# Kernel optimization log

Measured on AMD Instinct MI355X. Metric: run time of the kernel, lower is better.

The kernel has to match this reference:

```python
import jax, jax.numpy as jnp
import numpy as np

RADIUS = 0.1
NSAMPLE = 64
NEVENT = 2048
B, N, D = 4, 16384, 62
CHANNEL = D + 2  # 64


def index_events(events, idx):
    # events: [B, N, C], idx: [B, ...] -> [B, ..., C]
    return jax.vmap(lambda e, i: e[i])(events, idx)


def square_distance(src, dst):
    # src: [B, S, 2], dst: [B, N, 2] -> [B, S, N]
    return (jnp.sum(src ** 2, -1)[:, :, None]
            + jnp.sum(dst ** 2, -1)[:, None, :]
            - 2.0 * jnp.einsum('bsc,bnc->bsn', src, dst))


def research_circle(radius, nsample, xy, new_xy):
    n = xy.shape[1]
    sqrdists = square_distance(new_xy, xy)            # [B, S, N]
    ar = jnp.arange(n, dtype=jnp.int32)
    group_idx = jnp.where(sqrdists > radius ** 2, n, ar)  # out-of-ball -> N (sorts last)
    group_idx = jnp.sort(group_idx, axis=-1)[:, :, :nsample]
    first = group_idx[:, :, :1]
    return jnp.where(group_idx == n, first, group_idx)     # [B, S, nsample]


def reference(xy, events, fps_idx, affine_alpha, affine_beta):
    b, _, c = xy.shape
    new_xy = index_events(xy, fps_idx)                     # [B, S, 2]
    idx = research_circle(RADIUS, NSAMPLE, xy, new_xy)     # [B, S, K]
    grouped_xy = index_events(xy, idx)                     # [B, S, K, 2]
    grouped_events = index_events(events, idx)             # [B, S, K, D]
    # Normalize (normalize='center')
    g = jnp.concatenate([grouped_events, grouped_xy], axis=-1)  # [B, S, K, D+2]
    mean = jnp.mean(g, axis=2, keepdims=True)              # [B, S, 1, C]
    centered = g - mean
    std = jnp.std(centered.reshape(b, -1), axis=-1, ddof=1)[:, None, None, None]
    g = centered / (std + 1e-05)
    new_events = affine_alpha * g + affine_beta            # [B, S, K, 64]
    return new_xy, new_events


def setup_inputs() -> dict:
    key = jax.random.key(0)
    k1, k2, k3 = jax.random.split(key, 3)
    xy = jax.random.uniform(k1, (B, N, 2), dtype=jnp.float32)
    events = jax.random.normal(k2, (B, N, D), dtype=jnp.float32)
    fps_idx = jax.random.randint(k3, (B, NEVENT), 0, N, dtype=jnp.int32)
    affine_alpha = jnp.ones((1, 1, 1, CHANNEL), dtype=jnp.float32)
    affine_beta = jnp.zeros((1, 1, 1, CHANNEL), dtype=jnp.float32)
    return {"xy": xy, "events": events, "fps_idx": fps_idx,
            "affine_alpha": affine_alpha, "affine_beta": affine_beta}
```

## Files before the change

kernel.cpp:

```cpp
#include <hip/hip_runtime.h>
#include <stdint.h>
#include <math.h>

#define NPTS 16384
#define DEV 62
#define NEVENT 2048
#define NSAMPLE 64
#define CH 64
#define NBATCH 4
#define STOT (NBATCH * NEVENT)
#define M_PER_BATCH (NEVENT * NSAMPLE * CH)

#define OUT1_BASE 16384
#define REG_STRIDE (NSAMPLE * CH)
#define SL_MEAN 64
#define SL_INV 128
#define SL_SS 129

__global__ __launch_bounds__(256) void knn_kernel(
    const float2* __restrict__ xy,
    const int* __restrict__ fps,
    float* __restrict__ out)
{
    int wave = blockIdx.x * 4 + (threadIdx.x >> 6);
    int lane = threadIdx.x & 63;
    int b = wave >> 11;

    const float2* xyb = xy + b * NPTS;
    int qi = fps[wave];
    float2 q = xyb[qi];
    if (lane == 0) ((float2*)out)[wave] = q;

    float ssq = __fadd_rn(__fmul_rn(q.x, q.x), __fmul_rn(q.y, q.y));
    const float thr = 0.01f;

    int* regidx = (int*)(out + OUT1_BASE + (size_t)wave * REG_STRIDE);
    int m = 0;
    int first = -1;

    for (int base = 0; base < NPTS; base += 64) {
        float2 p = xyb[base + lane];
        float ssp = __fadd_rn(__fmul_rn(p.x, p.x), __fmul_rn(p.y, p.y));
        float dot = __builtin_fmaf(q.y, p.y, __fmul_rn(q.x, p.x));
        float d   = __fsub_rn(__fadd_rn(ssq, ssp), __fmul_rn(2.0f, dot));
        bool ok = !(d > thr);
        unsigned long long bal = __ballot(ok);
        if (first < 0 && bal != 0ull)
            first = base + (__ffsll((unsigned long long)bal) - 1);
        if (ok) {
            int pos = m + __popcll(bal & ((1ull << lane) - 1ull));
            if (pos < NSAMPLE) regidx[pos] = base + lane;
        }
        m += __popcll(bal);
        if (m >= NSAMPLE) break;
    }
    if (m < NSAMPLE) {
        for (int p = m + lane; p < NSAMPLE; p += 64)
            regidx[p] = first;
    }
}

__global__ __launch_bounds__(256) void stats_kernel(
    const float2* __restrict__ xy,
    const float* __restrict__ ev,
    float* __restrict__ out)
{
    int s = blockIdx.x;
    int b = s >> 11;
    int tid = threadIdx.x;
    float* reg = out + OUT1_BASE + (size_t)s * REG_STRIDE;

    __shared__ int sidx[NSAMPLE];
    __shared__ float ssum[2][256];
    __shared__ float smean[CH];
    __shared__ float swred[4];

    if (tid < NSAMPLE) sidx[tid] = ((const int*)reg)[tid];
    __syncthreads();

    int c2 = tid & 31;
    int kq = tid >> 5;

    const float* evb = ev + (size_t)b * NPTS * DEV;
    const float2* xyb = xy + b * NPTS;

    float g0[8], g1[8];
    float a0 = 0.f, a1 = 0.f;
#pragma unroll
    for (int j = 0; j < 8; ++j) {
        int row = sidx[8 * j + kq];
        float2 v;
        if (c2 < 31) v = *(const float2*)(evb + (size_t)row * DEV + 2 * c2);
        else         v = xyb[row];
        g0[j] = v.x; g1[j] = v.y;
        a0 += v.x;   a1 += v.y;
    }
    ssum[0][tid] = a0;
    ssum[1][tid] = a1;
    __syncthreads();

    if (tid < CH) {
        int which = tid >> 5, cc = tid & 31;
        float t = 0.f;
#pragma unroll
        for (int q = 0; q < 8; ++q) t += ssum[which][q * 32 + cc];
        smean[2 * cc + which] = t * (1.0f / NSAMPLE);
    }
    __syncthreads();

    if (tid < CH) reg[SL_MEAN + tid] = smean[tid];

    float m0 = smean[2 * c2], m1 = smean[2 * c2 + 1];
    float ss = 0.f;
#pragma unroll
    for (int j = 0; j < 8; ++j) {
        float c0 = g0[j] - m0;
        float c1 = g1[j] - m1;
        ss += c0 * c0 + c1 * c1;
    }

    for (int off = 32; off > 0; off >>= 1) ss += __shfl_down(ss, off, 64);
    if ((tid & 63) == 0) swred[tid >> 6] = ss;
    __syncthreads();
    if (tid == 0) reg[SL_SS] = swred[0] + swred[1] + swred[2] + swred[3];
}

__global__ __launch_bounds__(256) void reduce_std_kernel(float* __restrict__ out)
{
    int b = blockIdx.x;
    int tid = threadIdx.x;
    double acc = 0.0;
    for (int i = tid; i < NEVENT; i += 256)
        acc += (double)out[OUT1_BASE + (size_t)(b * NEVENT + i) * REG_STRIDE + SL_SS];
    __shared__ double sd[256];
    __shared__ float sinv;
    sd[tid] = acc;
    __syncthreads();
    for (int off = 128; off > 0; off >>= 1) {
        if (tid < off) sd[tid] += sd[tid + off];
        __syncthreads();
    }
    if (tid == 0) {
        double stdv = sqrt(sd[0] / (double)(M_PER_BATCH - 1));
        sinv = (float)(1.0 / (stdv + 1e-5));
    }
    __syncthreads();
    float inv = sinv;
    for (int i = tid; i < NEVENT; i += 256)
        out[OUT1_BASE + (size_t)(b * NEVENT + i) * REG_STRIDE + SL_INV] = inv;
}

__global__ __launch_bounds__(256) void finalize_kernel(
    const float2* __restrict__ xy,
    const float* __restrict__ ev,
    const float* __restrict__ alpha,
    const float* __restrict__ beta,
    float* __restrict__ out)
{
    int s = blockIdx.x;
    int b = s >> 11;
    int tid = threadIdx.x;
    float* reg = out + OUT1_BASE + (size_t)s * REG_STRIDE;

    __shared__ int sidx[NSAMPLE];
    __shared__ float sm[CH], sa[CH], sbet[CH];
    __shared__ float sinv;

    if (tid < NSAMPLE) {
        sidx[tid] = ((const int*)reg)[tid];
        sm[tid] = reg[SL_MEAN + tid];
    } else if (tid < 128) {
        sa[tid - 64] = alpha[tid - 64];
        sbet[tid - 64] = beta[tid - 64];
    } else if (tid == 128) {
        sinv = reg[SL_INV];
    }
    __syncthreads();

    int c2 = tid & 31;
    int kq = tid >> 5;
    float inv = sinv;

    const float* evb = ev + (size_t)b * NPTS * DEV;
    const float2* xyb = xy + b * NPTS;

    float m0 = sm[2 * c2],   m1 = sm[2 * c2 + 1];
    float al0 = sa[2 * c2],  al1 = sa[2 * c2 + 1];
    float be0 = sbet[2 * c2], be1 = sbet[2 * c2 + 1];

    float2* outp = (float2*)reg;
#pragma unroll
    for (int j = 0; j < 8; ++j) {
        int row = sidx[8 * j + kq];
        float2 v;
        if (c2 < 31) v = *(const float2*)(evb + (size_t)row * DEV + 2 * c2);
        else         v = xyb[row];
        float2 r;
        r.x = al0 * ((v.x - m0) * inv) + be0;
        r.y = al1 * ((v.y - m1) * inv) + be1;
        outp[256 * j + tid] = r;
    }
}

extern "C" void kernel_launch(void* const* d_in, const int* in_sizes, int n_in,
                              void* d_out, int out_size, void* d_ws, size_t ws_size,
                              hipStream_t stream) {
    const float2* xy    = (const float2*)d_in[0];
    const float*  ev    = (const float*)d_in[1];
    const int*    fps   = (const int*)d_in[2];
    const float*  alpha = (const float*)d_in[3];
    const float*  beta  = (const float*)d_in[4];
    float* out = (float*)d_out;
    (void)d_ws; (void)ws_size;

    knn_kernel<<<STOT / 4, 256, 0, stream>>>(xy, fps, out);
    stats_kernel<<<STOT, 256, 0, stream>>>(xy, ev, out);
    reduce_std_kernel<<<NBATCH, 256, 0, stream>>>(out);
    finalize_kernel<<<STOT, 256, 0, stream>>>(xy, ev, alpha, beta, out);
}
```

Baseline: 209.5 us.

## Fuse ball-query search into stats kernel and move scratch data to workspace

The neighbour search now runs in the first wave of each stats block and writes indices to shared memory, which removes a separate kernel launch and its global round-trip of indices. Per-query means, partial sums and the inverse std now live in a dedicated workspace instead of being scattered into the output buffer. The std reduction no longer broadcasts the inverse std to every query slot. The trade-off is that three of the four waves in each stats block sit idle during the serial search, which lowers occupancy for that phase compared with the old one-query-per-wave kernel.

```diff
diff --git a/kernel.cpp b/kernel.cpp
--- a/kernel.cpp
+++ b/kernel.cpp
@@ -12,77 +12,66 @@
 #define M_PER_BATCH (NEVENT * NSAMPLE * CH)
 
 #define OUT1_BASE 16384
-#define REG_STRIDE (NSAMPLE * CH)
-#define SL_MEAN 64
-#define SL_INV 128
-#define SL_SS 129
-
-__global__ __launch_bounds__(256) void knn_kernel(
-    const float2* __restrict__ xy,
-    const int* __restrict__ fps,
-    float* __restrict__ out)
-{
-    int wave = blockIdx.x * 4 + (threadIdx.x >> 6);
-    int lane = threadIdx.x & 63;
-    int b = wave >> 11;
-
-    const float2* xyb = xy + b * NPTS;
-    int qi = fps[wave];
-    float2 q = xyb[qi];
-    if (lane == 0) ((float2*)out)[wave] = q;
-
-    float ssq = __fadd_rn(__fmul_rn(q.x, q.x), __fmul_rn(q.y, q.y));
-    const float thr = 0.01f;
-
-    int* regidx = (int*)(out + OUT1_BASE + (size_t)wave * REG_STRIDE);
-    int m = 0;
-    int first = -1;
-
-    for (int base = 0; base < NPTS; base += 64) {
-        float2 p = xyb[base + lane];
-        float ssp = __fadd_rn(__fmul_rn(p.x, p.x), __fmul_rn(p.y, p.y));
-        float dot = __builtin_fmaf(q.y, p.y, __fmul_rn(q.x, p.x));
-        float d   = __fsub_rn(__fadd_rn(ssq, ssp), __fmul_rn(2.0f, dot));
-        bool ok = !(d > thr);
-        unsigned long long bal = __ballot(ok);
-        if (first < 0 && bal != 0ull)
-            first = base + (__ffsll((unsigned long long)bal) - 1);
-        if (ok) {
-            int pos = m + __popcll(bal & ((1ull << lane) - 1ull));
-            if (pos < NSAMPLE) regidx[pos] = base + lane;
-        }
-        m += __popcll(bal);
-        if (m >= NSAMPLE) break;
-    }
-    if (m < NSAMPLE) {
-        for (int p = m + lane; p < NSAMPLE; p += 64)
-            regidx[p] = first;
-    }
-}
-
-__global__ __launch_bounds__(256) void stats_kernel(
+
+__global__ __launch_bounds__(256) void knn_stats_kernel(
     const float2* __restrict__ xy,
     const float* __restrict__ ev,
-    float* __restrict__ out)
+    const int* __restrict__ fps,
+    float* __restrict__ out,
+    int* __restrict__ idx_ws,
+    float* __restrict__ mean_ws,
+    float* __restrict__ partial)
 {
     int s = blockIdx.x;
     int b = s >> 11;
     int tid = threadIdx.x;
-    float* reg = out + OUT1_BASE + (size_t)s * REG_STRIDE;
 
     __shared__ int sidx[NSAMPLE];
     __shared__ float ssum[2][256];
     __shared__ float smean[CH];
     __shared__ float swred[4];
 
-    if (tid < NSAMPLE) sidx[tid] = ((const int*)reg)[tid];
-    __syncthreads();
+    const float2* xyb = xy + b * NPTS;
+
+    if (tid < 64) {
+        int lane = tid;
+        int qi = fps[s];
+        float2 q = xyb[qi];
+        if (lane == 0) ((float2*)out)[s] = q;
+
+        float ssq = __fadd_rn(__fmul_rn(q.x, q.x), __fmul_rn(q.y, q.y));
+        const float thr = 0.01f;
+
+        int m = 0;
+        int first = -1;
+        for (int base = 0; base < NPTS; base += 64) {
+            float2 p = xyb[base + lane];
+            float ssp = __fadd_rn(__fmul_rn(p.x, p.x), __fmul_rn(p.y, p.y));
+            float dot = __builtin_fmaf(q.y, p.y, __fmul_rn(q.x, p.x));
+            float d   = __fsub_rn(__fadd_rn(ssq, ssp), __fmul_rn(2.0f, dot));
+            bool ok = !(d > thr);
+            unsigned long long bal = __ballot(ok);
+            if (first < 0 && bal != 0ull)
+                first = (int)(base + (__ffsll((unsigned long long)bal) - 1));
+            if (ok) {
+                int pos = m + __popcll(bal & ((1ull << lane) - 1ull));
+                if (pos < NSAMPLE) sidx[pos] = base + lane;
+            }
+            m += __popcll(bal);
+            if (m >= NSAMPLE) break;
+        }
+        if (m < NSAMPLE) {
+            for (int p = m + lane; p < NSAMPLE; p += 64)
+                sidx[p] = first;
+        }
+    }
+    __syncthreads();
+
+    if (tid < NSAMPLE) idx_ws[s * NSAMPLE + tid] = sidx[tid];
 
     int c2 = tid & 31;
     int kq = tid >> 5;
-
     const float* evb = ev + (size_t)b * NPTS * DEV;
-    const float2* xyb = xy + b * NPTS;
 
     float g0[8], g1[8];
     float a0 = 0.f, a1 = 0.f;
@@ -108,7 +97,7 @@
     }
     __syncthreads();
 
-    if (tid < CH) reg[SL_MEAN + tid] = smean[tid];
+    if (tid < CH) mean_ws[s * CH + tid] = smean[tid];
 
     float m0 = smean[2 * c2], m1 = smean[2 * c2 + 1];
     float ss = 0.f;
@@ -122,18 +111,18 @@
     for (int off = 32; off > 0; off >>= 1) ss += __shfl_down(ss, off, 64);
     if ((tid & 63) == 0) swred[tid >> 6] = ss;
     __syncthreads();
-    if (tid == 0) reg[SL_SS] = swred[0] + swred[1] + swred[2] + swred[3];
-}
-
-__global__ __launch_bounds__(256) void reduce_std_kernel(float* __restrict__ out)
+    if (tid == 0) partial[s] = swred[0] + swred[1] + swred[2] + swred[3];
+}
+
+__global__ __launch_bounds__(256) void reduce_std_kernel(
+    const float* __restrict__ partial, float* __restrict__ inv_std)
 {
     int b = blockIdx.x;
     int tid = threadIdx.x;
     double acc = 0.0;
     for (int i = tid; i < NEVENT; i += 256)
-        acc += (double)out[OUT1_BASE + (size_t)(b * NEVENT + i) * REG_STRIDE + SL_SS];
+        acc += (double)partial[b * NEVENT + i];
     __shared__ double sd[256];
-    __shared__ float sinv;
     sd[tid] = acc;
     __syncthreads();
     for (int off = 128; off > 0; off >>= 1) {
@@ -142,17 +131,16 @@
     }
     if (tid == 0) {
         double stdv = sqrt(sd[0] / (double)(M_PER_BATCH - 1));
-        sinv = (float)(1.0 / (stdv + 1e-5));
-    }
-    __syncthreads();
-    float inv = sinv;
-    for (int i = tid; i < NEVENT; i += 256)
-        out[OUT1_BASE + (size_t)(b * NEVENT + i) * REG_STRIDE + SL_INV] = inv;
+        inv_std[b] = (float)(1.0 / (stdv + 1e-5));
+    }
 }
 
 __global__ __launch_bounds__(256) void finalize_kernel(
     const float2* __restrict__ xy,
     const float* __restrict__ ev,
+    const int* __restrict__ idx_ws,
+    const float* __restrict__ mean_ws,
+    const float* __restrict__ inv_std,
     const float* __restrict__ alpha,
     const float* __restrict__ beta,
     float* __restrict__ out)
@@ -160,35 +148,31 @@
     int s = blockIdx.x;
     int b = s >> 11;
     int tid = threadIdx.x;
-    float* reg = out + OUT1_BASE + (size_t)s * REG_STRIDE;
 
     __shared__ int sidx[NSAMPLE];
     __shared__ float sm[CH], sa[CH], sbet[CH];
-    __shared__ float sinv;
 
     if (tid < NSAMPLE) {
-        sidx[tid] = ((const int*)reg)[tid];
-        sm[tid] = reg[SL_MEAN + tid];
+        sidx[tid] = idx_ws[s * NSAMPLE + tid];
+        sm[tid] = mean_ws[s * CH + tid];
     } else if (tid < 128) {
         sa[tid - 64] = alpha[tid - 64];
         sbet[tid - 64] = beta[tid - 64];
-    } else if (tid == 128) {
-        sinv = reg[SL_INV];
     }
     __syncthreads();
 
     int c2 = tid & 31;
     int kq = tid >> 5;
-    float inv = sinv;
+    float inv = inv_std[b];
 
     const float* evb = ev + (size_t)b * NPTS * DEV;
     const float2* xyb = xy + b * NPTS;
 
-    float m0 = sm[2 * c2],   m1 = sm[2 * c2 + 1];
-    float al0 = sa[2 * c2],  al1 = sa[2 * c2 + 1];
+    float m0 = sm[2 * c2],    m1 = sm[2 * c2 + 1];
+    float al0 = sa[2 * c2],   al1 = sa[2 * c2 + 1];
     float be0 = sbet[2 * c2], be1 = sbet[2 * c2 + 1];
 
-    float2* outp = (float2*)reg;
+    float2* outp = (float2*)(out + OUT1_BASE + (size_t)s * (NSAMPLE * CH));
 #pragma unroll
     for (int j = 0; j < 8; ++j) {
         int row = sidx[8 * j + kq];
@@ -211,10 +195,15 @@
     const float*  alpha = (const float*)d_in[3];
     const float*  beta  = (const float*)d_in[4];
     float* out = (float*)d_out;
-    (void)d_ws; (void)ws_size;
-
-    knn_kernel<<<STOT / 4, 256, 0, stream>>>(xy, fps, out);
-    stats_kernel<<<STOT, 256, 0, stream>>>(xy, ev, out);
-    reduce_std_kernel<<<NBATCH, 256, 0, stream>>>(out);
-    finalize_kernel<<<STOT, 256, 0, stream>>>(xy, ev, alpha, beta, out);
-}
+
+    int*   idx_ws  = (int*)d_ws;
+    float* mean_ws = (float*)(idx_ws + STOT * NSAMPLE);
+    float* partial = mean_ws + STOT * CH;
+    float* inv_std = partial + STOT;
+
+    knn_stats_kernel<<<STOT, 256, 0, stream>>>(xy, ev, fps, out,
+                                               idx_ws, mean_ws, partial);
+    reduce_std_kernel<<<NBATCH, 256, 0, stream>>>(partial, inv_std);
+    finalize_kernel<<<STOT, 256, 0, stream>>>(xy, ev, idx_ws, mean_ws, inv_std,
+                                              alpha, beta, out);
+}
```

Result: slower. 236.8 us (+13.0%).
